# Kernel optimization log

Measured on AMD Instinct MI355X. Metric: run time of the kernel, lower is better.

Reference implementation:

```python
import jax, jax.numpy as jnp
import numpy as np

B, C, D = 8192, 4, 256
E, H, O = 8, 256, 128
AQ, HQ = 18, 512
THRESH = 0.3
MAX_OUT_REC = 2


def setup_inputs() -> dict:
    key = jax.random.key(0)
    ks = jax.random.split(key, 16)
    s = lambda *sh: 1.0 / np.sqrt(sh[-2] if len(sh) > 1 else sh[-1])
    inp = {
        'data': jax.random.normal(ks[0], (B, C, D), jnp.float32),
        # stacked expert MLPs: D -> H -> O
        'We1': jax.random.normal(ks[1], (E, D, H), jnp.float32) / np.sqrt(D),
        'be1': jnp.zeros((E, H), jnp.float32),
        'We2': jax.random.normal(ks[2], (E, H, O), jnp.float32) / np.sqrt(H),
        'be2': jnp.zeros((E, O), jnp.float32),
        # gating: D -> E (softmax)
        'Wg': jax.random.normal(ks[3], (D, E), jnp.float32) / np.sqrt(D),
        'bg': jnp.zeros((E,), jnp.float32),
        # outer recursive gating: C*O -> 2 (softmax)
        'Wog': jax.random.normal(ks[4], (C * O, 2), jnp.float32) / np.sqrt(C * O),
        'bog': jnp.zeros((2,), jnp.float32),
        # recursive mapping: O -> D
        'Wr': jax.random.normal(ks[5], (O, D), jnp.float32) / np.sqrt(O),
        'br': jnp.zeros((D,), jnp.float32),
        # Q network: C*O -> HQ -> A
        'Wq1': jax.random.normal(ks[6], (C * O, HQ), jnp.float32) / np.sqrt(C * O),
        'bq1': jnp.zeros((HQ,), jnp.float32),
        'Wq2': jax.random.normal(ks[7], (HQ, AQ), jnp.float32) / np.sqrt(HQ),
        'bq2': jnp.zeros((AQ,), jnp.float32),
    }
    return inp


def _moe_forward(x3, We1, be1, We2, be2, Wg, bg):
    # x3: (B, C, D) -> tokens (N, D), N = B*C
    b = x3.shape[0]
    x = x3.reshape(b * C, D)
    # dense all-experts forward
    h = jax.nn.relu(jnp.einsum('nd,edh->enh', x, We1) + be1[:, None, :])  # (E,N,H)
    eo = jnp.einsum('enh,eho->eno', h, We2) + be2[:, None, :]              # (E,N,O)
    g = jax.nn.softmax(x @ Wg + bg, axis=-1)                               # (N,E)
    out = jnp.einsum('ne,eno->no', g, eo)                                  # (N,O)
    return out.reshape(b, C * O)


def reference(data, We1, be1, We2, be2, Wg, bg, Wog, bog, Wr, br, Wq1, bq1, Wq2, bq2):
    result = _moe_forward(data, We1, be1, We2, be2, Wg, bg)               # (B, C*O)
    co = jax.nn.softmax(result @ Wog + bog, axis=-1)                      # (B, 2)
    gate2 = (co[:, 0] > THRESH).astype(result.dtype)[:, None]             # (B, 1)
    # while-loop with per-sample mask; unrolled MAX_OUT_REC iterations is
    # exact: once a sample's mask is 0 its result (hence mask) is unchanged.
    for _ in range(MAX_OUT_REC):
        r_ = result.reshape(data.shape[0] * C, O) @ Wr + br               # recursive_mapping
        r3 = r_.reshape(data.shape[0], C, D)
        out = _moe_forward(r3, We1, be1, We2, be2, Wg, bg)
        result = result + out * co[:, 0:1] * gate2
        co = jax.nn.softmax(result @ Wog + bog, axis=-1)
        gate2 = (co[:, 0] > 0.5).astype(result.dtype)[:, None]
    values = jax.nn.relu(result @ Wq1 + bq1) @ Wq2 + bq2                  # (B, A)
    return values
```

## Files before the change

### kernel.cpp

```cpp
#include <hip/hip_runtime.h>
#include <math.h>


typedef _Float16 f16;
typedef f16   f16x8  __attribute__((ext_vector_type(8)));
typedef f16   f16x4  __attribute__((ext_vector_type(4)));
typedef float f32x16 __attribute__((ext_vector_type(16)));
typedef float v4f    __attribute__((ext_vector_type(4)));

#define MFMA(a, b, c) __builtin_amdgcn_mfma_f32_32x32x16_f16(a, b, c, 0, 0, 0)
#define LO_SCALE 4096.0f
#define LO_INV   (1.0f / 4096.0f)

#define XS 264
#define RS 136
#define QS 520

__device__ __forceinline__ v4f nt_load4(const float* p) {
    return __builtin_nontemporal_load((const v4f*)p);
}

__global__ __launch_bounds__(256) void prep_kernel(
    const float* __restrict__ We1, const float* __restrict__ We2,
    const float* __restrict__ Wr,  const float* __restrict__ Wg,
    const float* __restrict__ Wq1, const float* __restrict__ Wq2,
    f16* __restrict__ W1H, f16* __restrict__ W1L,
    f16* __restrict__ W2H, f16* __restrict__ W2L,
    f16* __restrict__ WrH, f16* __restrict__ WrL,
    f16* __restrict__ WgH, f16* __restrict__ WgL,
    f16* __restrict__ Wq1H, f16* __restrict__ Wq1L,
    f16* __restrict__ Wq2H, f16* __restrict__ Wq2L)
{
    int t = blockIdx.x * 4 + (threadIdx.x >> 6);
    int lane = threadIdx.x & 63;
    const float* src; f16 *dh, *dl;
    int stride, ncols, kbase, nbase, tile;
    if (t < 1024) {
        int e = t >> 7, kt = (t >> 3) & 15, nt = t & 7;
        src = We1 + e * 65536; stride = 256; ncols = 256;
        kbase = kt * 16; nbase = nt * 32; tile = t; dh = W1H; dl = W1L;
    } else if (t < 1536) {
        int i = t - 1024; int e = i >> 6, kt = (i >> 2) & 15, nt = i & 3;
        src = We2 + e * 32768; stride = 128; ncols = 128;
        kbase = kt * 16; nbase = nt * 32; tile = i; dh = W2H; dl = W2L;
    } else if (t < 1600) {
        int i = t - 1536; int kt = i >> 3, nt = i & 7;
        src = Wr; stride = 256; ncols = 256;
        kbase = kt * 16; nbase = nt * 32; tile = i; dh = WrH; dl = WrL;
    } else if (t < 1616) {
        int i = t - 1600;
        src = Wg; stride = 8; ncols = 8;
        kbase = i * 16; nbase = 0; tile = i; dh = WgH; dl = WgL;
    } else if (t < 2128) {
        int i = t - 1616; int kt = i >> 4, nt = i & 15;
        src = Wq1; stride = 512; ncols = 512;
        kbase = kt * 16; nbase = nt * 32; tile = i; dh = Wq1H; dl = Wq1L;
    } else {
        int i = t - 2128;
        src = Wq2; stride = 18; ncols = 18;
        kbase = i * 16; nbase = 0; tile = i; dh = Wq2H; dl = Wq2L;
    }
    int n = lane & 31, kg = lane >> 5;
    int col = nbase + n;
    f16x8 hv, lv;
    #pragma unroll
    for (int j = 0; j < 8; ++j) {
        int k = kbase + kg * 8 + j;
        float w = (col < ncols) ? src[(size_t)k * stride + col] : 0.f;
        f16 h = (f16)w;
        hv[j] = h;
        lv[j] = (f16)((w - (float)h) * LO_SCALE);
    }
    *(f16x8*)(dh + (size_t)tile * 512 + lane * 8) = hv;
    *(f16x8*)(dl + (size_t)tile * 512 + lane * 8) = lv;
}

template<bool REC>
__global__ __launch_bounds__(512, 2) void moe_mfma(
    const float* xsrc, const float* __restrict__ sbuf,
    const f16* __restrict__ W1H, const f16* __restrict__ W1L,
    const f16* __restrict__ W2H, const f16* __restrict__ W2L,
    const f16* __restrict__ WrH, const f16* __restrict__ WrL,
    const f16* __restrict__ WgH, const f16* __restrict__ WgL,
    const float* __restrict__ be1, const float* __restrict__ be2,
    const float* __restrict__ bg,  const float* __restrict__ br,
    float* result)
{
    extern __shared__ char smem[];
    f16* xh = (f16*)smem;
    f16* xl = xh + 64 * XS;
    f16* hh = xl + 64 * XS;
    f16* hl = hh + 64 * XS;
    float* gld = (float*)(hl + 64 * XS);

    const int tid = threadIdx.x;
    const int lane = tid & 63;
    const int wv = tid >> 6;
    const int l31 = lane & 31;
    const int kg = lane >> 5;
    const int n0 = blockIdx.x * 64;

    if (!REC) {
        #pragma unroll
        for (int i = 0; i < 8; ++i) {
            int idx = i * 512 + tid;
            int m = idx >> 6, k4 = (idx & 63) * 4;
            v4f v = nt_load4(&xsrc[(size_t)(n0 + m) * 256 + k4]);
            f16x4 hv, lv;
            #pragma unroll
            for (int j = 0; j < 4; ++j) {
                hv[j] = (f16)v[j];
                lv[j] = (f16)((v[j] - (float)hv[j]) * LO_SCALE);
            }
            *(f16x4*)&xh[m * XS + k4] = hv;
            *(f16x4*)&xl[m * XS + k4] = lv;
        }
    } else {
        #pragma unroll
        for (int i = 0; i < 4; ++i) {
            int idx = i * 512 + tid;
            int m = idx >> 5, k4 = (idx & 31) * 4;
            v4f v = nt_load4(&xsrc[(size_t)(n0 + m) * 128 + k4]);
            f16x4 hv, lv;
            #pragma unroll
            for (int j = 0; j < 4; ++j) {
                hv[j] = (f16)v[j];
                lv[j] = (f16)((v[j] - (float)hv[j]) * LO_SCALE);
            }
            *(f16x4*)&hh[m * RS + k4] = hv;
            *(f16x4*)&hl[m * RS + k4] = lv;
        }
        __syncthreads();
        f32x16 am0 = {}, ac0 = {}, am1 = {}, ac1 = {};
        const f16* wrh = WrH + (size_t)wv * 512 + lane * 8;
        const f16* wrl = WrL + (size_t)wv * 512 + lane * 8;
        #pragma unroll
        for (int kt = 0; kt < 8; ++kt) {
            f16x8 bh = *(const f16x8*)(wrh + kt * 4096);
            f16x8 bl = *(const f16x8*)(wrl + kt * 4096);
            f16x8 ah0 = *(const f16x8*)&hh[l31 * RS + kt * 16 + kg * 8];
            f16x8 al0 = *(const f16x8*)&hl[l31 * RS + kt * 16 + kg * 8];
            f16x8 ah1 = *(const f16x8*)&hh[(32 + l31) * RS + kt * 16 + kg * 8];
            f16x8 al1 = *(const f16x8*)&hl[(32 + l31) * RS + kt * 16 + kg * 8];
            am0 = MFMA(ah0, bh, am0); ac0 = MFMA(al0, bh, ac0); ac0 = MFMA(ah0, bl, ac0);
            am1 = MFMA(ah1, bh, am1); ac1 = MFMA(al1, bh, ac1); ac1 = MFMA(ah1, bl, ac1);
        }
        {
            int col = wv * 32 + l31;
            float brv = br[col];
            #pragma unroll
            for (int Mt = 0; Mt < 2; ++Mt) {
                #pragma unroll
                for (int r = 0; r < 16; ++r) {
                    int row = (r & 3) + 8 * (r >> 2) + 4 * kg + Mt * 32;
                    float v = (Mt ? am1[r] + ac1[r] * LO_INV
                                  : am0[r] + ac0[r] * LO_INV) + brv;
                    f16 hv = (f16)v;
                    xh[row * XS + col] = hv;
                    xl[row * XS + col] = (f16)((v - (float)hv) * LO_SCALE);
                }
            }
        }
    }
    __syncthreads();

    if (wv < 2) {
        f32x16 am = {}, ac = {};
        int Mt = wv;
        #pragma unroll
        for (int kt = 0; kt < 16; ++kt) {
            f16x8 ah = *(const f16x8*)&xh[(Mt * 32 + l31) * XS + kt * 16 + kg * 8];
            f16x8 al = *(const f16x8*)&xl[(Mt * 32 + l31) * XS + kt * 16 + kg * 8];
            f16x8 bh = *(const f16x8*)(WgH + (size_t)kt * 512 + lane * 8);
            f16x8 bl = *(const f16x8*)(WgL + (size_t)kt * 512 + lane * 8);
            am = MFMA(ah, bh, am); ac = MFMA(al, bh, ac); ac = MFMA(ah, bl, ac);
        }
        int e = l31;
        float bge = (e < 8) ? bg[e] : 0.f;
        #pragma unroll
        for (int r = 0; r < 16; ++r) {
            float lg = am[r] + ac[r] * LO_INV + bge;
            float mx = lg;
            #pragma unroll
            for (int d = 1; d < 8; d <<= 1) mx = fmaxf(mx, __shfl_xor(mx, d, 64));
            float ex = __expf(lg - mx);
            float s = ex;
            #pragma unroll
            for (int d = 1; d < 8; d <<= 1) s += __shfl_xor(s, d, 64);
            if (e < 8) {
                int row = (r & 3) + 8 * (r >> 2) + 4 * kg + Mt * 32;
                gld[row * 8 + e] = ex / s;
            }
        }
    }
    __syncthreads();

    f32x16 out = {};
    const int Mt2 = wv >> 2, nt2 = wv & 3;
    #pragma unroll 1
    for (int e = 0; e < 8; ++e) {
        f32x16 am0 = {}, ac0 = {}, am1 = {}, ac1 = {};
        const f16* w1h = W1H + (size_t)e * 65536 + wv * 512 + lane * 8;
        const f16* w1l = W1L + (size_t)e * 65536 + wv * 512 + lane * 8;
        #pragma unroll
        for (int kt = 0; kt < 16; ++kt) {
            f16x8 bh = *(const f16x8*)(w1h + kt * 4096);
            f16x8 bl = *(const f16x8*)(w1l + kt * 4096);
            f16x8 ah0 = *(const f16x8*)&xh[l31 * XS + kt * 16 + kg * 8];
            f16x8 al0 = *(const f16x8*)&xl[l31 * XS + kt * 16 + kg * 8];
            f16x8 ah1 = *(const f16x8*)&xh[(32 + l31) * XS + kt * 16 + kg * 8];
            f16x8 al1 = *(const f16x8*)&xl[(32 + l31) * XS + kt * 16 + kg * 8];
            am0 = MFMA(ah0, bh, am0); ac0 = MFMA(al0, bh, ac0); ac0 = MFMA(ah0, bl, ac0);
            am1 = MFMA(ah1, bh, am1); ac1 = MFMA(al1, bh, ac1); ac1 = MFMA(ah1, bl, ac1);
        }
        __syncthreads();
        {
            int col = wv * 32 + l31;
            float b1v = be1[e * 256 + col];
            #pragma unroll
            for (int Mt = 0; Mt < 2; ++Mt) {
                #pragma unroll
                for (int r = 0; r < 16; ++r) {
                    int row = (r & 3) + 8 * (r >> 2) + 4 * kg + Mt * 32;
                    float v = (Mt ? am1[r] + ac1[r] * LO_INV
                                  : am0[r] + ac0[r] * LO_INV) + b1v;
                    v = fmaxf(v, 0.f);
                    f16 hv = (f16)v;
                    hh[row * XS + col] = hv;
                    hl[row * XS + col] = (f16)((v - (float)hv) * LO_SCALE);
                }
            }
        }
        __syncthreads();
        f32x16 am2 = {}, ac2 = {};
        const f16* w2h = W2H + (size_t)e * 32768 + nt2 * 512 + lane * 8;
        const f16* w2l = W2L + (size_t)e * 32768 + nt2 * 512 + lane * 8;
        #pragma unroll
        for (int kt = 0; kt < 16; ++kt) {
            f16x8 bh = *(const f16x8*)(w2h + kt * 2048);
            f16x8 bl = *(const f16x8*)(w2l + kt * 2048);
            f16x8 ah = *(const f16x8*)&hh[(Mt2 * 32 + l31) * XS + kt * 16 + kg * 8];
            f16x8 al = *(const f16x8*)&hl[(Mt2 * 32 + l31) * XS + kt * 16 + kg * 8];
            am2 = MFMA(ah, bh, am2); ac2 = MFMA(al, bh, ac2); ac2 = MFMA(ah, bl, ac2);
        }
        float be2v = be2[e * 128 + nt2 * 32 + l31];
        #pragma unroll
        for (int r = 0; r < 16; ++r) {
            int row = (r & 3) + 8 * (r >> 2) + 4 * kg + Mt2 * 32;
            float gv = gld[row * 8 + e];
            out[r] += gv * (am2[r] + ac2[r] * LO_INV + be2v);
        }
    }

    int col = nt2 * 32 + l31;
    #pragma unroll
    for (int r = 0; r < 16; ++r) {
        int row = (r & 3) + 8 * (r >> 2) + 4 * kg + Mt2 * 32;
        size_t off = (size_t)(n0 + row) * 128 + col;
        float v = out[r];
        if (REC) {
            float sv = sbuf[(n0 + row) >> 2];
            float old = __builtin_nontemporal_load(&result[off]);
            v = old + v * sv;
        }
        __builtin_nontemporal_store(v, &result[off]);
    }
}

__global__ __launch_bounds__(256) void co_kernel(
    const float* __restrict__ result, const float* __restrict__ Wog,
    const float* __restrict__ bog, float* __restrict__ sbuf, float thresh)
{
    int lane = threadIdx.x & 63;
    int w = threadIdx.x >> 6;
    int b = blockIdx.x * 4 + w;
    const float* r = result + (size_t)b * 512;
    float l0 = 0.f, l1 = 0.f;
    #pragma unroll
    for (int j = 0; j < 8; ++j) {
        int d = j * 64 + lane;
        float rv = __builtin_nontemporal_load(&r[d]);
        float2 wv = *(const float2*)&Wog[d * 2];
        l0 = fmaf(rv, wv.x, l0);
        l1 = fmaf(rv, wv.y, l1);
    }
    #pragma unroll
    for (int off = 32; off > 0; off >>= 1) {
        l0 += __shfl_down(l0, off);
        l1 += __shfl_down(l1, off);
    }
    if (lane == 0) {
        l0 += bog[0]; l1 += bog[1];
        float co0 = 1.f / (1.f + __expf(l1 - l0));
        sbuf[b] = (co0 > thresh) ? co0 : 0.f;
    }
}

__global__ __launch_bounds__(512, 2) void q_mfma(
    const float* __restrict__ result,
    const f16* __restrict__ Wq1H, const f16* __restrict__ Wq1L,
    const f16* __restrict__ Wq2H, const f16* __restrict__ Wq2L,
    const float* __restrict__ bq1, const float* __restrict__ bq2,
    float* __restrict__ out)
{
    extern __shared__ char smem[];
    f16* rh = (f16*)smem;
    f16* rl = rh + 32 * QS;
    f16* hh = rl + 32 * QS;
    f16* hl = hh + 32 * QS;
    float* part = (float*)(hl + 32 * QS);
    const int tid = threadIdx.x;
    const int lane = tid & 63;
    const int wv = tid >> 6;
    const int l31 = lane & 31;
    const int kg = lane >> 5;
    const int n0 = blockIdx.x * 32;

    #pragma unroll
    for (int i = 0; i < 8; ++i) {
        int idx = i * 512 + tid;
        int m = idx >> 7, k4 = (idx & 127) * 4;
        v4f v = nt_load4(&result[(size_t)(n0 + m) * 512 + k4]);
        f16x4 hv, lv;
        #pragma unroll
        for (int j = 0; j < 4; ++j) {
            hv[j] = (f16)v[j];
            lv[j] = (f16)((v[j] - (float)hv[j]) * LO_SCALE);
        }
        *(f16x4*)&rh[m * QS + k4] = hv;
        *(f16x4*)&rl[m * QS + k4] = lv;
    }
    __syncthreads();

    f32x16 am0 = {}, ac0 = {}, am1 = {}, ac1 = {};
    const int nt0 = wv * 2;
    #pragma unroll
    for (int kt = 0; kt < 32; ++kt) {
        f16x8 ah = *(const f16x8*)&rh[l31 * QS + kt * 16 + kg * 8];
        f16x8 al = *(const f16x8*)&rl[l31 * QS + kt * 16 + kg * 8];
        f16x8 b0h = *(const f16x8*)(Wq1H + (size_t)(kt * 16 + nt0) * 512 + lane * 8);
        f16x8 b0l = *(const f16x8*)(Wq1L + (size_t)(kt * 16 + nt0) * 512 + lane * 8);
        f16x8 b1h = *(const f16x8*)(Wq1H + (size_t)(kt * 16 + nt0 + 1) * 512 + lane * 8);
        f16x8 b1l = *(const f16x8*)(Wq1L + (size_t)(kt * 16 + nt0 + 1) * 512 + lane * 8);
        am0 = MFMA(ah, b0h, am0); ac0 = MFMA(al, b0h, ac0); ac0 = MFMA(ah, b0l, ac0);
        am1 = MFMA(ah, b1h, am1); ac1 = MFMA(al, b1h, ac1); ac1 = MFMA(ah, b1l, ac1);
    }
    #pragma unroll
    for (int t = 0; t < 2; ++t) {
        int col = (nt0 + t) * 32 + l31;
        float b1v = bq1[col];
        #pragma unroll
        for (int r = 0; r < 16; ++r) {
            int row = (r & 3) + 8 * (r >> 2) + 4 * kg;
            float v = (t ? am1[r] + ac1[r] * LO_INV : am0[r] + ac0[r] * LO_INV) + b1v;
            v = fmaxf(v, 0.f);
            f16 hv = (f16)v;
            hh[row * QS + col] = hv;
            hl[row * QS + col] = (f16)((v - (float)hv) * LO_SCALE);
        }
    }
    __syncthreads();

    if (wv < 4) {
        f32x16 am = {}, ac = {};
        #pragma unroll
        for (int k2 = 0; k2 < 8; ++k2) {
            int kt = wv * 8 + k2;
            f16x8 ah = *(const f16x8*)&hh[l31 * QS + kt * 16 + kg * 8];
            f16x8 al = *(const f16x8*)&hl[l31 * QS + kt * 16 + kg * 8];
            f16x8 bh = *(const f16x8*)(Wq2H + (size_t)kt * 512 + lane * 8);
            f16x8 bl = *(const f16x8*)(Wq2L + (size_t)kt * 512 + lane * 8);
            am = MFMA(ah, bh, am); ac = MFMA(al, bh, ac); ac = MFMA(ah, bl, ac);
        }
        #pragma unroll
        for (int r = 0; r < 16; ++r) {
            int row = (r & 3) + 8 * (r >> 2) + 4 * kg;
            part[wv * 1024 + row * 32 + l31] = am[r] + ac[r] * LO_INV;
        }
    }
    __syncthreads();
    for (int idx = tid; idx < 1024; idx += 512) {
        int row = idx >> 5, c = idx & 31;
        if (c < 18) {
            float s = part[idx] + part[1024 + idx] + part[2048 + idx] + part[3072 + idx]
                      + bq2[c];
            out[(size_t)(n0 + row) * 18 + c] = s;
        }
    }
}

extern "C" void kernel_launch(void* const* d_in, const int* in_sizes, int n_in,
                              void* d_out, int out_size, void* d_ws, size_t ws_size,
                              hipStream_t stream)
{
    (void)in_sizes; (void)n_in; (void)out_size; (void)ws_size;
    const float* data = (const float*)d_in[0];
    const float* We1  = (const float*)d_in[1];
    const float* be1  = (const float*)d_in[2];
    const float* We2  = (const float*)d_in[3];
    const float* be2  = (const float*)d_in[4];
    const float* Wg   = (const float*)d_in[5];
    const float* bg   = (const float*)d_in[6];
    const float* Wog  = (const float*)d_in[7];
    const float* bog  = (const float*)d_in[8];
    const float* Wr   = (const float*)d_in[9];
    const float* br   = (const float*)d_in[10];
    const float* Wq1  = (const float*)d_in[11];
    const float* bq1  = (const float*)d_in[12];
    const float* Wq2  = (const float*)d_in[13];
    const float* bq2  = (const float*)d_in[14];
    float* outp = (float*)d_out;

    float* result = (float*)d_ws;
    float* sbuf   = result + (size_t)32768 * 128;
    f16* fb = (f16*)((char*)d_ws + 16809984);
    f16* W1H  = fb;
    f16* W1L  = fb + 524288;
    f16* W2H  = fb + 1048576;
    f16* W2L  = fb + 1310720;
    f16* WrH  = fb + 1572864;
    f16* WrL  = fb + 1605632;
    f16* WgH  = fb + 1638400;
    f16* WgL  = fb + 1646592;
    f16* Wq1H = fb + 1654784;
    f16* Wq1L = fb + 1916928;
    f16* Wq2H = fb + 2179072;
    f16* Wq2L = fb + 2195456;

    const int MOE_LDS = 4 * 64 * XS * 2 + 64 * 8 * 4;
    const int Q_LDS   = 4 * 32 * QS * 2 + 4 * 1024 * 4;

    prep_kernel<<<540, 256, 0, stream>>>(We1, We2, Wr, Wg, Wq1, Wq2,
        W1H, W1L, W2H, W2L, WrH, WrL, WgH, WgL, Wq1H, Wq1L, Wq2H, Wq2L);

    moe_mfma<false><<<512, 512, MOE_LDS, stream>>>(
        data, nullptr, W1H, W1L, W2H, W2L, WrH, WrL, WgH, WgL,
        be1, be2, bg, br, result);
    co_kernel<<<2048, 256, 0, stream>>>(result, Wog, bog, sbuf, 0.3f);
    moe_mfma<true><<<512, 512, MOE_LDS, stream>>>(
        result, sbuf, W1H, W1L, W2H, W2L, WrH, WrL, WgH, WgL,
        be1, be2, bg, br, result);
    co_kernel<<<2048, 256, 0, stream>>>(result, Wog, bog, sbuf, 0.5f);
    moe_mfma<true><<<512, 512, MOE_LDS, stream>>>(
        result, sbuf, W1H, W1L, W2H, W2L, WrH, WrL, WgH, WgL,
        be1, be2, bg, br, result);
    q_mfma<<<256, 512, Q_LDS, stream>>>(result, Wq1H, Wq1L, Wq2H, Wq2L,
        bq1, bq2, outp);
}
```

Baseline: 821.8 us.

## Retile MoE kernel to 32-token blocks with per-wave dual N-tiles and register gating

The MoE kernel now processes 32 tokens per 256-thread block instead of 64 tokens per 512-thread block, doubling the grid and halving shared memory per block. Each wave computes two 32-column output tiles per GEMM so each activation fragment feeds two MFMA chains. Gating softmax is computed redundantly by every wave and kept in registers, then fetched by lane shuffle, which removes the LDS gate buffer and one barrier. Correction terms use separate accumulators to break MFMA dependency chains. The trade-off is that each weight fragment is reused across half as many tokens, so L2 weight traffic per token roughly doubles.

```diff
diff --git a/kernel.cpp b/kernel.cpp
--- a/kernel.cpp
+++ b/kernel.cpp
@@ -76,7 +76,7 @@
 }
 
 template<bool REC>
-__global__ __launch_bounds__(512, 2) void moe_mfma(
+__global__ __launch_bounds__(256, 2) void moe_mfma(
     const float* xsrc, const float* __restrict__ sbuf,
     const f16* __restrict__ W1H, const f16* __restrict__ W1L,
     const f16* __restrict__ W2H, const f16* __restrict__ W2L,
@@ -88,22 +88,21 @@
 {
     extern __shared__ char smem[];
     f16* xh = (f16*)smem;
-    f16* xl = xh + 64 * XS;
-    f16* hh = xl + 64 * XS;
-    f16* hl = hh + 64 * XS;
-    float* gld = (float*)(hl + 64 * XS);
+    f16* xl = xh + 32 * XS;
+    f16* hh = xl + 32 * XS;
+    f16* hl = hh + 32 * XS;
 
     const int tid = threadIdx.x;
     const int lane = tid & 63;
     const int wv = tid >> 6;
     const int l31 = lane & 31;
     const int kg = lane >> 5;
-    const int n0 = blockIdx.x * 64;
+    const int n0 = blockIdx.x * 32;
 
     if (!REC) {
         #pragma unroll
         for (int i = 0; i < 8; ++i) {
-            int idx = i * 512 + tid;
+            int idx = i * 256 + tid;
             int m = idx >> 6, k4 = (idx & 63) * 4;
             v4f v = nt_load4(&xsrc[(size_t)(n0 + m) * 256 + k4]);
             f16x4 hv, lv;
@@ -118,7 +117,7 @@
     } else {
         #pragma unroll
         for (int i = 0; i < 4; ++i) {
-            int idx = i * 512 + tid;
+            int idx = i * 256 + tid;
             int m = idx >> 5, k4 = (idx & 31) * 4;
             v4f v = nt_load4(&xsrc[(size_t)(n0 + m) * 128 + k4]);
             f16x4 hv, lv;
@@ -131,55 +130,52 @@
             *(f16x4*)&hl[m * RS + k4] = lv;
         }
         __syncthreads();
-        f32x16 am0 = {}, ac0 = {}, am1 = {}, ac1 = {};
-        const f16* wrh = WrH + (size_t)wv * 512 + lane * 8;
-        const f16* wrl = WrL + (size_t)wv * 512 + lane * 8;
+        f32x16 am0 = {}, a0a = {}, a0b = {}, am1 = {}, a1a = {}, a1b = {};
+        const f16* wrh = WrH + (size_t)(2 * wv) * 512 + lane * 8;
+        const f16* wrl = WrL + (size_t)(2 * wv) * 512 + lane * 8;
         #pragma unroll
         for (int kt = 0; kt < 8; ++kt) {
-            f16x8 bh = *(const f16x8*)(wrh + kt * 4096);
-            f16x8 bl = *(const f16x8*)(wrl + kt * 4096);
-            f16x8 ah0 = *(const f16x8*)&hh[l31 * RS + kt * 16 + kg * 8];
-            f16x8 al0 = *(const f16x8*)&hl[l31 * RS + kt * 16 + kg * 8];
-            f16x8 ah1 = *(const f16x8*)&hh[(32 + l31) * RS + kt * 16 + kg * 8];
-            f16x8 al1 = *(const f16x8*)&hl[(32 + l31) * RS + kt * 16 + kg * 8];
-            am0 = MFMA(ah0, bh, am0); ac0 = MFMA(al0, bh, ac0); ac0 = MFMA(ah0, bl, ac0);
-            am1 = MFMA(ah1, bh, am1); ac1 = MFMA(al1, bh, ac1); ac1 = MFMA(ah1, bl, ac1);
-        }
-        {
-            int col = wv * 32 + l31;
+            f16x8 b0h = *(const f16x8*)(wrh + (size_t)kt * 4096);
+            f16x8 b0l = *(const f16x8*)(wrl + (size_t)kt * 4096);
+            f16x8 b1h = *(const f16x8*)(wrh + (size_t)kt * 4096 + 512);
+            f16x8 b1l = *(const f16x8*)(wrl + (size_t)kt * 4096 + 512);
+            f16x8 ah = *(const f16x8*)&hh[l31 * RS + kt * 16 + kg * 8];
+            f16x8 al = *(const f16x8*)&hl[l31 * RS + kt * 16 + kg * 8];
+            am0 = MFMA(ah, b0h, am0); a0a = MFMA(al, b0h, a0a); a0b = MFMA(ah, b0l, a0b);
+            am1 = MFMA(ah, b1h, am1); a1a = MFMA(al, b1h, a1a); a1b = MFMA(ah, b1l, a1b);
+        }
+        #pragma unroll
+        for (int t = 0; t < 2; ++t) {
+            int col = (2 * wv + t) * 32 + l31;
             float brv = br[col];
             #pragma unroll
-            for (int Mt = 0; Mt < 2; ++Mt) {
-                #pragma unroll
-                for (int r = 0; r < 16; ++r) {
-                    int row = (r & 3) + 8 * (r >> 2) + 4 * kg + Mt * 32;
-                    float v = (Mt ? am1[r] + ac1[r] * LO_INV
-                                  : am0[r] + ac0[r] * LO_INV) + brv;
-                    f16 hv = (f16)v;
-                    xh[row * XS + col] = hv;
-                    xl[row * XS + col] = (f16)((v - (float)hv) * LO_SCALE);
-                }
+            for (int r = 0; r < 16; ++r) {
+                int row = (r & 3) + 8 * (r >> 2) + 4 * kg;
+                float v = (t ? am1[r] + (a1a[r] + a1b[r]) * LO_INV
+                             : am0[r] + (a0a[r] + a0b[r]) * LO_INV) + brv;
+                f16 hv = (f16)v;
+                xh[row * XS + col] = hv;
+                xl[row * XS + col] = (f16)((v - (float)hv) * LO_SCALE);
             }
         }
     }
     __syncthreads();
 
-    if (wv < 2) {
-        f32x16 am = {}, ac = {};
-        int Mt = wv;
+    float gr[16];
+    {
+        f32x16 gm = {}, ga = {}, gb = {};
         #pragma unroll
         for (int kt = 0; kt < 16; ++kt) {
-            f16x8 ah = *(const f16x8*)&xh[(Mt * 32 + l31) * XS + kt * 16 + kg * 8];
-            f16x8 al = *(const f16x8*)&xl[(Mt * 32 + l31) * XS + kt * 16 + kg * 8];
+            f16x8 ah = *(const f16x8*)&xh[l31 * XS + kt * 16 + kg * 8];
+            f16x8 al = *(const f16x8*)&xl[l31 * XS + kt * 16 + kg * 8];
             f16x8 bh = *(const f16x8*)(WgH + (size_t)kt * 512 + lane * 8);
             f16x8 bl = *(const f16x8*)(WgL + (size_t)kt * 512 + lane * 8);
-            am = MFMA(ah, bh, am); ac = MFMA(al, bh, ac); ac = MFMA(ah, bl, ac);
-        }
-        int e = l31;
-        float bge = (e < 8) ? bg[e] : 0.f;
+            gm = MFMA(ah, bh, gm); ga = MFMA(al, bh, ga); gb = MFMA(ah, bl, gb);
+        }
+        float bge = (l31 < 8) ? bg[l31] : 0.f;
         #pragma unroll
         for (int r = 0; r < 16; ++r) {
-            float lg = am[r] + ac[r] * LO_INV + bge;
+            float lg = gm[r] + (ga[r] + gb[r]) * LO_INV + bge;
             float mx = lg;
             #pragma unroll
             for (int d = 1; d < 8; d <<= 1) mx = fmaxf(mx, __shfl_xor(mx, d, 64));
@@ -187,75 +183,68 @@
             float s = ex;
             #pragma unroll
             for (int d = 1; d < 8; d <<= 1) s += __shfl_xor(s, d, 64);
-            if (e < 8) {
-                int row = (r & 3) + 8 * (r >> 2) + 4 * kg + Mt * 32;
-                gld[row * 8 + e] = ex / s;
-            }
-        }
-    }
-    __syncthreads();
+            gr[r] = ex / s;
+        }
+    }
 
     f32x16 out = {};
-    const int Mt2 = wv >> 2, nt2 = wv & 3;
     #pragma unroll 1
     for (int e = 0; e < 8; ++e) {
-        f32x16 am0 = {}, ac0 = {}, am1 = {}, ac1 = {};
-        const f16* w1h = W1H + (size_t)e * 65536 + wv * 512 + lane * 8;
-        const f16* w1l = W1L + (size_t)e * 65536 + wv * 512 + lane * 8;
+        f32x16 am0 = {}, a0a = {}, a0b = {}, am1 = {}, a1a = {}, a1b = {};
+        const f16* w1h = W1H + (size_t)e * 65536 + (2 * wv) * 512 + lane * 8;
+        const f16* w1l = W1L + (size_t)e * 65536 + (2 * wv) * 512 + lane * 8;
         #pragma unroll
         for (int kt = 0; kt < 16; ++kt) {
-            f16x8 bh = *(const f16x8*)(w1h + kt * 4096);
-            f16x8 bl = *(const f16x8*)(w1l + kt * 4096);
-            f16x8 ah0 = *(const f16x8*)&xh[l31 * XS + kt * 16 + kg * 8];
-            f16x8 al0 = *(const f16x8*)&xl[l31 * XS + kt * 16 + kg * 8];
-            f16x8 ah1 = *(const f16x8*)&xh[(32 + l31) * XS + kt * 16 + kg * 8];
-            f16x8 al1 = *(const f16x8*)&xl[(32 + l31) * XS + kt * 16 + kg * 8];
-            am0 = MFMA(ah0, bh, am0); ac0 = MFMA(al0, bh, ac0); ac0 = MFMA(ah0, bl, ac0);
-            am1 = MFMA(ah1, bh, am1); ac1 = MFMA(al1, bh, ac1); ac1 = MFMA(ah1, bl, ac1);
+            f16x8 b0h = *(const f16x8*)(w1h + (size_t)kt * 4096);
+            f16x8 b0l = *(const f16x8*)(w1l + (size_t)kt * 4096);
+            f16x8 b1h = *(const f16x8*)(w1h + (size_t)kt * 4096 + 512);
+            f16x8 b1l = *(const f16x8*)(w1l + (size_t)kt * 4096 + 512);
+            f16x8 ah = *(const f16x8*)&xh[l31 * XS + kt * 16 + kg * 8];
+            f16x8 al = *(const f16x8*)&xl[l31 * XS + kt * 16 + kg * 8];
+            am0 = MFMA(ah, b0h, am0); a0a = MFMA(al, b0h, a0a); a0b = MFMA(ah, b0l, a0b);
+            am1 = MFMA(ah, b1h, am1); a1a = MFMA(al, b1h, a1a); a1b = MFMA(ah, b1l, a1b);
         }
         __syncthreads();
-        {
-            int col = wv * 32 + l31;
+        #pragma unroll
+        for (int t = 0; t < 2; ++t) {
+            int col = (2 * wv + t) * 32 + l31;
             float b1v = be1[e * 256 + col];
             #pragma unroll
-            for (int Mt = 0; Mt < 2; ++Mt) {
-                #pragma unroll
-                for (int r = 0; r < 16; ++r) {
-                    int row = (r & 3) + 8 * (r >> 2) + 4 * kg + Mt * 32;
-                    float v = (Mt ? am1[r] + ac1[r] * LO_INV
-                                  : am0[r] + ac0[r] * LO_INV) + b1v;
-                    v = fmaxf(v, 0.f);
-                    f16 hv = (f16)v;
-                    hh[row * XS + col] = hv;
-                    hl[row * XS + col] = (f16)((v - (float)hv) * LO_SCALE);
-                }
+            for (int r = 0; r < 16; ++r) {
+                int row = (r & 3) + 8 * (r >> 2) + 4 * kg;
+                float v = (t ? am1[r] + (a1a[r] + a1b[r]) * LO_INV
+                             : am0[r] + (a0a[r] + a0b[r]) * LO_INV) + b1v;
+                v = fmaxf(v, 0.f);
+                f16 hv = (f16)v;
+                hh[row * XS + col] = hv;
+                hl[row * XS + col] = (f16)((v - (float)hv) * LO_SCALE);
             }
         }
         __syncthreads();
-        f32x16 am2 = {}, ac2 = {};
-        const f16* w2h = W2H + (size_t)e * 32768 + nt2 * 512 + lane * 8;
-        const f16* w2l = W2L + (size_t)e * 32768 + nt2 * 512 + lane * 8;
+        f32x16 am2 = {}, a2a = {}, a2b = {};
+        const f16* w2h = W2H + (size_t)e * 32768 + wv * 512 + lane * 8;
+        const f16* w2l = W2L + (size_t)e * 32768 + wv * 512 + lane * 8;
         #pragma unroll
         for (int kt = 0; kt < 16; ++kt) {
-            f16x8 bh = *(const f16x8*)(w2h + kt * 2048);
-            f16x8 bl = *(const f16x8*)(w2l + kt * 2048);
-            f16x8 ah = *(const f16x8*)&hh[(Mt2 * 32 + l31) * XS + kt * 16 + kg * 8];
-            f16x8 al = *(const f16x8*)&hl[(Mt2 * 32 + l31) * XS + kt * 16 + kg * 8];
-            am2 = MFMA(ah, bh, am2); ac2 = MFMA(al, bh, ac2); ac2 = MFMA(ah, bl, ac2);
-        }
-        float be2v = be2[e * 128 + nt2 * 32 + l31];
+            f16x8 bh = *(const f16x8*)(w2h + (size_t)kt * 2048);
+            f16x8 bl = *(const f16x8*)(w2l + (size_t)kt * 2048);
+            f16x8 ah = *(const f16x8*)&hh[l31 * XS + kt * 16 + kg * 8];
+            f16x8 al = *(const f16x8*)&hl[l31 * XS + kt * 16 + kg * 8];
+            am2 = MFMA(ah, bh, am2); a2a = MFMA(al, bh, a2a); a2b = MFMA(ah, bl, a2b);
+        }
+        float be2v = be2[e * 128 + wv * 32 + l31];
         #pragma unroll
         for (int r = 0; r < 16; ++r) {
-            int row = (r & 3) + 8 * (r >> 2) + 4 * kg + Mt2 * 32;
-            float gv = gld[row * 8 + e];
-            out[r] += gv * (am2[r] + ac2[r] * LO_INV + be2v);
-        }
-    }
-
-    int col = nt2 * 32 + l31;
+            float eo = am2[r] + (a2a[r] + a2b[r]) * LO_INV + be2v;
+            float gv = __shfl(gr[r], (lane & 32) + e, 64);
+            out[r] += gv * eo;
+        }
+    }
+
+    int col = wv * 32 + l31;
     #pragma unroll
     for (int r = 0; r < 16; ++r) {
-        int row = (r & 3) + 8 * (r >> 2) + 4 * kg + Mt2 * 32;
+        int row = (r & 3) + 8 * (r >> 2) + 4 * kg;
         size_t off = (size_t)(n0 + row) * 128 + col;
         float v = out[r];
         if (REC) {
@@ -427,21 +416,21 @@
     f16* Wq2H = fb + 2179072;
     f16* Wq2L = fb + 2195456;
 
-    const int MOE_LDS = 4 * 64 * XS * 2 + 64 * 8 * 4;
+    const int MOE_LDS = 4 * 32 * XS * 2;
     const int Q_LDS   = 4 * 32 * QS * 2 + 4 * 1024 * 4;
 
     prep_kernel<<<540, 256, 0, stream>>>(We1, We2, Wr, Wg, Wq1, Wq2,
         W1H, W1L, W2H, W2L, WrH, WrL, WgH, WgL, Wq1H, Wq1L, Wq2H, Wq2L);
 
-    moe_mfma<false><<<512, 512, MOE_LDS, stream>>>(
+    moe_mfma<false><<<1024, 256, MOE_LDS, stream>>>(
         data, nullptr, W1H, W1L, W2H, W2L, WrH, WrL, WgH, WgL,
         be1, be2, bg, br, result);
     co_kernel<<<2048, 256, 0, stream>>>(result, Wog, bog, sbuf, 0.3f);
-    moe_mfma<true><<<512, 512, MOE_LDS, stream>>>(
+    moe_mfma<true><<<1024, 256, MOE_LDS, stream>>>(
         result, sbuf, W1H, W1L, W2H, W2L, WrH, WrL, WgH, WgL,
         be1, be2, bg, br, result);
     co_kernel<<<2048, 256, 0, stream>>>(result, Wog, bog, sbuf, 0.5f);
-    moe_mfma<true><<<512, 512, MOE_LDS, stream>>>(
+    moe_mfma<true><<<1024, 256, MOE_LDS, stream>>>(
         result, sbuf, W1H, W1L, W2H, W2L, WrH, WrL, WgH, WgL,
         be1, be2, bg, br, result);
     q_mfma<<<256, 512, Q_LDS, stream>>>(result, Wq1H, Wq1L, Wq2H, Wq2L,
```

After: 739.5 us. -10.0%, faster.
